# Optimization experiments

Measured on AMD Instinct MI355X. Metric: run time of the kernel, lower is better.

Reference implementation:

```python
import jax, jax.numpy as jnp
import numpy as np

DIMS = (8, 8, 16, 16)   # 4D lattice, X = prod(DIMS) = 16384
KS = 2                  # kernel_size
DIL = 0                 # dilation
NC = 3                  # SU(3)
N_IN = 4
N_OUT = 8
T_W_SIZE = N_IN * (2 * (KS - 1) * len(DIMS) + 1) + 1  # 37 (includes unit element)
BATCH = 4
X = int(np.prod(DIMS))


def complex_einsum(pattern, a, b, conj_a=1, conj_b=1):
    # last axis of a, b is (real, imag)
    aR, aI = a[..., 0], conj_a * a[..., 1]
    bR, bI = b[..., 0], conj_b * b[..., 1]
    cR = jnp.einsum(pattern, aR, bR) - jnp.einsum(pattern, aI, bI)
    cI = jnp.einsum(pattern, aR, bI) + jnp.einsum(pattern, aI, bR)
    return jnp.stack((cR, cI), axis=-1)


def shift(a, axis, orientation):
    # roll the flattened lattice dim X along lattice axis `axis`
    s = a.shape
    a_l = a.reshape((s[0],) + DIMS + s[2:])
    return jnp.roll(a_l, orientation, axis=axis + 1).reshape(s)


def transport(u, w, axis, orientation):
    ws = shift(w, axis, -orientation)
    ua = u[:, :, axis]  # (b, X, nc, nc, 2)
    if orientation > 0:
        wt = complex_einsum('bxij,bxwjk->bxwik', ua, ws)
        wt = complex_einsum('bxwij,bxkj->bxwik', wt, ua, conj_b=-1)
    else:
        ua = shift(ua, axis, +1)
        wt = complex_einsum('bxji,bxwjk->bxwik', ua, ws, conj_a=-1)
        wt = complex_einsum('bxwij,bxjk->bxwik', wt, ua)
    return wt


def setup_inputs() -> dict:
    key = jax.random.key(0)
    k1, k2, k3 = jax.random.split(key, 3)
    u = jax.random.normal(k1, (BATCH, X, len(DIMS), NC, NC, 2), dtype=jnp.float32)
    w = jax.random.normal(k2, (BATCH, X, N_IN, NC, NC, 2), dtype=jnp.float32)
    std = 1.0 * float(np.sqrt(1.0 / T_W_SIZE))
    weight = std * jax.random.normal(k3, (N_OUT, T_W_SIZE), dtype=jnp.float32)
    return {"u": u, "w": w, "weight": weight}


def reference(u, w, weight):
    terms = [w]
    for orientation in (+1, -1):
        for axis in range(len(DIMS)):
            wt = w
            for d in range(1, KS):
                for step in range(DIL + 1):
                    wt = transport(u, wt, axis=axis, orientation=orientation)
                terms.append(wt)
    t_w = jnp.concatenate(terms, axis=2)  # (b, X, n_in*(2*(ks-1)*ndim+1), nc, nc, 2)
    # append unit (identity) element channel
    unit = jnp.stack((jnp.eye(NC, dtype=t_w.dtype), jnp.zeros((NC, NC), dtype=t_w.dtype)), axis=-1)
    unit_t = jnp.broadcast_to(unit, (t_w.shape[0], t_w.shape[1], 1, NC, NC, 2))
    t_w = jnp.concatenate((t_w, unit_t), axis=2)  # (b, X, T_W_SIZE, nc, nc, 2)
    w_out = jnp.einsum('uv,bxvijc->bxuijc', weight, t_w)
    return (u, w_out)
```

## Files before the change

kernel.cpp:

```cpp
#include <hip/hip_runtime.h>

namespace {

constexpr int NCOL  = 3;
constexpr int N_IN  = 4;
constexpr int N_OUT = 8;
constexpr int T_W   = 37;
constexpr int NB    = 4;
constexpr int NX    = 16384;
constexpr int MAT   = 18;
constexpr int NSJ   = NB * NX * 3;
constexpr int NTHREADS = NSJ * 2;
constexpr int OUT_U = NB * NX * 4 * MAT;

__device__ constexpr int SH[4] = {11, 8, 4, 0};
__device__ constexpr int DD[4] = {8, 8, 16, 16};
__device__ constexpr int SS[4] = {2048, 256, 16, 1};

template<int PAR>
__device__ __forceinline__ void load_mat18(const float* __restrict__ p, float* M) {
    if constexpr (PAR == 0) {
        float4 q0 = *(const float4*)(p + 0);
        float4 q1 = *(const float4*)(p + 4);
        float4 q2 = *(const float4*)(p + 8);
        float4 q3 = *(const float4*)(p + 12);
        float2 q4 = *(const float2*)(p + 16);
        M[0]=q0.x;  M[1]=q0.y;  M[2]=q0.z;  M[3]=q0.w;
        M[4]=q1.x;  M[5]=q1.y;  M[6]=q1.z;  M[7]=q1.w;
        M[8]=q2.x;  M[9]=q2.y;  M[10]=q2.z; M[11]=q2.w;
        M[12]=q3.x; M[13]=q3.y; M[14]=q3.z; M[15]=q3.w;
        M[16]=q4.x; M[17]=q4.y;
    } else {
        float2 q4 = *(const float2*)(p + 0);
        float4 q0 = *(const float4*)(p + 2);
        float4 q1 = *(const float4*)(p + 6);
        float4 q2 = *(const float4*)(p + 10);
        float4 q3 = *(const float4*)(p + 14);
        M[0]=q4.x;  M[1]=q4.y;
        M[2]=q0.x;  M[3]=q0.y;  M[4]=q0.z;  M[5]=q0.w;
        M[6]=q1.x;  M[7]=q1.y;  M[8]=q1.z;  M[9]=q1.w;
        M[10]=q2.x; M[11]=q2.y; M[12]=q2.z; M[13]=q2.w;
        M[14]=q3.x; M[15]=q3.y; M[16]=q3.z; M[17]=q3.w;
    }
}

template<int O>
__device__ __forceinline__ void transport_col(
    const float U[18], const float vr[3], const float vi[3],
    const float W[18], float cr[3], float ci[3])
{
    float yr[3], yi[3];
#pragma unroll
    for (int i = 0; i < 3; ++i) {
        float sr = 0.f, si = 0.f;
#pragma unroll
        for (int k = 0; k < 3; ++k) {
            float wr = W[(i*3+k)*2], wi = W[(i*3+k)*2+1];
            sr = fmaf(wr, vr[k], sr); sr = fmaf(-wi, vi[k], sr);
            si = fmaf(wr, vi[k], si); si = fmaf(wi, vr[k], si);
        }
        yr[i] = sr; yi[i] = si;
    }
#pragma unroll
    for (int i = 0; i < 3; ++i) {
        float sr = 0.f, si = 0.f;
#pragma unroll
        for (int k = 0; k < 3; ++k) {
            if constexpr (O == 0) {
                float ur = U[(i*3+k)*2], ui = U[(i*3+k)*2+1];
                sr = fmaf(ur, yr[k], sr); sr = fmaf(-ui, yi[k], sr);
                si = fmaf(ur, yi[k], si); si = fmaf(ui, yr[k], si);
            } else {
                float ur = U[(k*3+i)*2], ui = U[(k*3+i)*2+1];
                sr = fmaf(ur, yr[k], sr); sr = fmaf(ui, yi[k], sr);
                si = fmaf(ur, yi[k], si); si = fmaf(-ui, yr[k], si);
            }
        }
        cr[i] = sr; ci[i] = si;
    }
}

__device__ __forceinline__ void mix(const float (*wT)[N_OUT], int ch,
    const float cr[3], const float ci[3], float acc[N_OUT][NCOL][2])
{
    float4 lo = *(const float4*)&wT[ch][0];
    float4 hi = *(const float4*)&wT[ch][4];
    const float cw[8] = {lo.x, lo.y, lo.z, lo.w, hi.x, hi.y, hi.z, hi.w};
#pragma unroll
    for (int uo = 0; uo < 8; ++uo)
#pragma unroll
        for (int i = 0; i < 3; ++i) {
            acc[uo][i][0] = fmaf(cw[uo], cr[i], acc[uo][i][0]);
            acc[uo][i][1] = fmaf(cw[uo], ci[i], acc[uo][i][1]);
        }
}

template<int O>
__device__ __forceinline__ void do_orientation(
    int x, int bs, int j,
    const float* __restrict__ u, const float* __restrict__ w,
    const float (*wT)[N_OUT], float acc[N_OUT][NCOL][2])
{
#pragma unroll
    for (int a = 0; a < 4; ++a) {
        const int ca = (x >> SH[a]) & (DD[a] - 1);
        int xn;
        if constexpr (O == 0) xn = (ca == DD[a]-1) ? x - (DD[a]-1)*SS[a] : x + SS[a];
        else                  xn = (ca == 0)       ? x + (DD[a]-1)*SS[a] : x - SS[a];
        const int bsn = bs - x + xn;
        const int us  = (O == 0) ? bs : bsn;

        const float* __restrict__ Up = u + (size_t)us * (4 * MAT) + a * MAT;
        float U[18];
        if ((a & 1) == 0) load_mat18<0>(Up, U);
        else              load_mat18<1>(Up, U);

        float vr[3], vi[3];
#pragma unroll
        for (int k = 0; k < 3; ++k) {
            const int eidx = (O == 0) ? (j*3 + k) : (k*3 + j);
            float2 e = *(const float2*)(Up + eidx * 2);
            vr[k] = e.x;
            vi[k] = (O == 0) ? -e.y : e.y;
        }

        const float* __restrict__ wn = w + (size_t)bsn * (N_IN * MAT);
        const int chbase = ((O == 0) ? (1 + a) : (5 + a)) * 4;

        float WA[18], WB[18], cr[3], ci[3];
        load_mat18<0>(wn + 0 * MAT, WA);
        load_mat18<1>(wn + 1 * MAT, WB);

        transport_col<O>(U, vr, vi, WA, cr, ci);
        mix(wT, chbase + 0, cr, ci, acc);
        load_mat18<0>(wn + 2 * MAT, WA);

        transport_col<O>(U, vr, vi, WB, cr, ci);
        mix(wT, chbase + 1, cr, ci, acc);
        load_mat18<1>(wn + 3 * MAT, WB);

        transport_col<O>(U, vr, vi, WA, cr, ci);
        mix(wT, chbase + 2, cr, ci, acc);

        transport_col<O>(U, vr, vi, WB, cr, ci);
        mix(wT, chbase + 3, cr, ci, acc);
    }
}

__global__ __launch_bounds__(256) void lconv_kernel(
    const float* __restrict__ u,
    const float* __restrict__ w,
    const float* __restrict__ wgt,
    float* __restrict__ out)
{
    __shared__ float  wT[T_W][N_OUT];
    __shared__ float2 red[256][13];

    const int tid = threadIdx.x;
    for (int idx = tid; idx < T_W * N_OUT; idx += 256) {
        int uo = idx & 7;
        int v  = idx >> 3;
        wT[v][uo] = wgt[uo * T_W + v];
    }
    __syncthreads();

    const int gid = blockIdx.x * 256 + tid;

    {
        const float4* __restrict__ u4 = (const float4*)u;
        float4* __restrict__ o4 = (float4*)out;
#pragma unroll
        for (int k = 0; k < 3; ++k) {
            int idx = gid + k * NTHREADS;
            o4[idx] = u4[idx];
        }
    }

    const int o  = tid >> 7;
    const int sj = blockIdx.x * 128 + (tid & 127);
    const int j  = sj % 3;
    const int bs = sj / 3;
    const int x  = bs & (NX - 1);

    const float* __restrict__ wbase = w + (size_t)bs * (N_IN * MAT);

    float acc[N_OUT][NCOL][2];
#pragma unroll
    for (int uo = 0; uo < N_OUT; ++uo)
#pragma unroll
        for (int i = 0; i < NCOL; ++i) { acc[uo][i][0] = 0.f; acc[uo][i][1] = 0.f; }

#pragma unroll
    for (int t = 0; t < 2; ++t) {
        const int v = 2 * o + t;
        float4 lo = *(const float4*)&wT[v][0];
        float4 hi = *(const float4*)&wT[v][4];
        const float cw[8] = {lo.x, lo.y, lo.z, lo.w, hi.x, hi.y, hi.z, hi.w};
#pragma unroll
        for (int i = 0; i < NCOL; ++i) {
            float2 e = *(const float2*)(wbase + v * MAT + (i * NCOL + j) * 2);
#pragma unroll
            for (int uo = 0; uo < N_OUT; ++uo) {
                acc[uo][i][0] = fmaf(cw[uo], e.x, acc[uo][i][0]);
                acc[uo][i][1] = fmaf(cw[uo], e.y, acc[uo][i][1]);
            }
        }
    }

    if (o == 0) do_orientation<0>(x, bs, j, u, w, wT, acc);
    else        do_orientation<1>(x, bs, j, u, w, wT, acc);

    if (o == 0) {
#pragma unroll
        for (int t = 0; t < 4; ++t)
#pragma unroll
            for (int i = 0; i < 3; ++i)
                red[tid][t * 3 + i] = make_float2(acc[4 + t][i][0], acc[4 + t][i][1]);
    } else {
#pragma unroll
        for (int t = 0; t < 4; ++t)
#pragma unroll
            for (int i = 0; i < 3; ++i)
                red[tid][t * 3 + i] = make_float2(acc[t][i][0], acc[t][i][1]);
    }
    __syncthreads();

    const int partner = tid ^ 128;
    float* __restrict__ obase = out + (size_t)OUT_U + (size_t)bs * (N_OUT * MAT);
    float4 idq = *(const float4*)&wT[36][4 * o];
    const float cid[4] = {idq.x, idq.y, idq.z, idq.w};

    if (o == 0) {
#pragma unroll
        for (int t = 0; t < 4; ++t)
#pragma unroll
            for (int i = 0; i < 3; ++i) {
                float2 r = red[partner][t * 3 + i];
                float2 e;
                e.x = acc[t][i][0] + r.x + ((i == j) ? cid[t] : 0.f);
                e.y = acc[t][i][1] + r.y;
                *(float2*)(obase + t * MAT + (i * NCOL + j) * 2) = e;
            }
    } else {
#pragma unroll
        for (int t = 0; t < 4; ++t)
#pragma unroll
            for (int i = 0; i < 3; ++i) {
                float2 r = red[partner][t * 3 + i];
                float2 e;
                e.x = acc[4 + t][i][0] + r.x + ((i == j) ? cid[t] : 0.f);
                e.y = acc[4 + t][i][1] + r.y;
                *(float2*)(obase + (4 + t) * MAT + (i * NCOL + j) * 2) = e;
            }
    }
}

}

extern "C" void kernel_launch(void* const* d_in, const int* in_sizes, int n_in,
                              void* d_out, int out_size, void* d_ws, size_t ws_size,
                              hipStream_t stream)
{
    const float* u   = (const float*)d_in[0];
    const float* w   = (const float*)d_in[1];
    const float* wgt = (const float*)d_in[2];
    float* out = (float*)d_out;

    dim3 block(256);
    dim3 grid(NTHREADS / 256);
    lconv_kernel<<<grid, block, 0, stream>>>(u, w, wgt, out);
}
```

Baseline: 57.23 us.

## Remap threads so each wavefront handles one column across 64 sites

Blocks grow to 384 threads covering 64 sites. Each wavefront now owns one (orientation, column) pair, so the column index and orientation are uniform within a wavefront and the branching on j no longer diverges. The column vector for the link matrix is now taken from the matrix already held in registers instead of being reloaded from memory. The cross-orientation reduction uses a smaller shared buffer and is done in two phases with extra barriers, which adds synchronisation. Per-lane loads of neighbouring sites become more contiguous.

```diff
diff --git a/kernel.cpp b/kernel.cpp
--- a/kernel.cpp
+++ b/kernel.cpp
@@ -9,9 +9,11 @@
 constexpr int NB    = 4;
 constexpr int NX    = 16384;
 constexpr int MAT   = 18;
-constexpr int NSJ   = NB * NX * 3;
-constexpr int NTHREADS = NSJ * 2;
-constexpr int OUT_U = NB * NX * 4 * MAT;
+constexpr int SITES = NB * NX;
+constexpr int BLK   = 384;
+constexpr int NBLK  = SITES / 64;
+constexpr int NTHREADS = NBLK * BLK;
+constexpr int OUT_U = SITES * 4 * MAT;
 
 __device__ constexpr int SH[4] = {11, 8, 4, 0};
 __device__ constexpr int DD[4] = {8, 8, 16, 16};
@@ -44,6 +46,15 @@
     }
 }
 
+template<int O, int J>
+__device__ __forceinline__ void extract_d(const float U[18], float vr[3], float vi[3]) {
+#pragma unroll
+    for (int k = 0; k < 3; ++k) {
+        if constexpr (O == 0) { vr[k] = U[(J*3+k)*2]; vi[k] = -U[(J*3+k)*2+1]; }
+        else                  { vr[k] = U[(k*3+J)*2]; vi[k] =  U[(k*3+J)*2+1]; }
+    }
+}
+
 template<int O>
 __device__ __forceinline__ void transport_col(
     const float U[18], const float vr[3], const float vi[3],
@@ -116,13 +127,9 @@
         else              load_mat18<1>(Up, U);
 
         float vr[3], vi[3];
-#pragma unroll
-        for (int k = 0; k < 3; ++k) {
-            const int eidx = (O == 0) ? (j*3 + k) : (k*3 + j);
-            float2 e = *(const float2*)(Up + eidx * 2);
-            vr[k] = e.x;
-            vi[k] = (O == 0) ? -e.y : e.y;
-        }
+        if      (j == 0) extract_d<O, 0>(U, vr, vi);
+        else if (j == 1) extract_d<O, 1>(U, vr, vi);
+        else             extract_d<O, 2>(U, vr, vi);
 
         const float* __restrict__ wn = w + (size_t)bsn * (N_IN * MAT);
         const int chbase = ((O == 0) ? (1 + a) : (5 + a)) * 4;
@@ -147,24 +154,22 @@
     }
 }
 
-__global__ __launch_bounds__(256) void lconv_kernel(
+__global__ __launch_bounds__(BLK) void lconv_kernel(
     const float* __restrict__ u,
     const float* __restrict__ w,
     const float* __restrict__ wgt,
     float* __restrict__ out)
 {
     __shared__ float  wT[T_W][N_OUT];
-    __shared__ float2 red[256][13];
+    __shared__ float2 red[192][13];
 
     const int tid = threadIdx.x;
-    for (int idx = tid; idx < T_W * N_OUT; idx += 256) {
-        int uo = idx & 7;
-        int v  = idx >> 3;
-        wT[v][uo] = wgt[uo * T_W + v];
-    }
-    __syncthreads();
-
-    const int gid = blockIdx.x * 256 + tid;
+    for (int idx = tid; idx < T_W * N_OUT; idx += BLK) {
+        wT[idx >> 3][idx & 7] = wgt[(idx & 7) * T_W + (idx >> 3)];
+    }
+    __syncthreads();
+
+    const int gid = blockIdx.x * BLK + tid;
 
     {
         const float4* __restrict__ u4 = (const float4*)u;
@@ -176,11 +181,12 @@
         }
     }
 
-    const int o  = tid >> 7;
-    const int sj = blockIdx.x * 128 + (tid & 127);
-    const int j  = sj % 3;
-    const int bs = sj / 3;
-    const int x  = bs & (NX - 1);
+    const int wv   = tid >> 6;
+    const int lane = tid & 63;
+    const int o    = (wv >= 3) ? 1 : 0;
+    const int j    = wv - 3 * o;
+    const int bs   = blockIdx.x * 64 + lane;
+    const int x    = bs & (NX - 1);
 
     const float* __restrict__ wbase = w + (size_t)bs * (N_IN * MAT);
 
@@ -210,43 +216,47 @@
     if (o == 0) do_orientation<0>(x, bs, j, u, w, wT, acc);
     else        do_orientation<1>(x, bs, j, u, w, wT, acc);
 
-    if (o == 0) {
-#pragma unroll
-        for (int t = 0; t < 4; ++t)
-#pragma unroll
-            for (int i = 0; i < 3; ++i)
-                red[tid][t * 3 + i] = make_float2(acc[4 + t][i][0], acc[4 + t][i][1]);
-    } else {
-#pragma unroll
-        for (int t = 0; t < 4; ++t)
-#pragma unroll
-            for (int i = 0; i < 3; ++i)
-                red[tid][t * 3 + i] = make_float2(acc[t][i][0], acc[t][i][1]);
-    }
-    __syncthreads();
-
-    const int partner = tid ^ 128;
+    const int p = tid - 192 * o;
     float* __restrict__ obase = out + (size_t)OUT_U + (size_t)bs * (N_OUT * MAT);
     float4 idq = *(const float4*)&wT[36][4 * o];
     const float cid[4] = {idq.x, idq.y, idq.z, idq.w};
 
+    if (o == 1) {
+#pragma unroll
+        for (int t = 0; t < 4; ++t)
+#pragma unroll
+            for (int i = 0; i < 3; ++i)
+                red[p][t * 3 + i] = make_float2(acc[t][i][0], acc[t][i][1]);
+    }
+    __syncthreads();
     if (o == 0) {
 #pragma unroll
         for (int t = 0; t < 4; ++t)
 #pragma unroll
             for (int i = 0; i < 3; ++i) {
-                float2 r = red[partner][t * 3 + i];
+                float2 r = red[p][t * 3 + i];
                 float2 e;
                 e.x = acc[t][i][0] + r.x + ((i == j) ? cid[t] : 0.f);
                 e.y = acc[t][i][1] + r.y;
                 *(float2*)(obase + t * MAT + (i * NCOL + j) * 2) = e;
             }
-    } else {
+    }
+    __syncthreads();
+
+    if (o == 0) {
+#pragma unroll
+        for (int t = 0; t < 4; ++t)
+#pragma unroll
+            for (int i = 0; i < 3; ++i)
+                red[p][t * 3 + i] = make_float2(acc[4 + t][i][0], acc[4 + t][i][1]);
+    }
+    __syncthreads();
+    if (o == 1) {
 #pragma unroll
         for (int t = 0; t < 4; ++t)
 #pragma unroll
             for (int i = 0; i < 3; ++i) {
-                float2 r = red[partner][t * 3 + i];
+                float2 r = red[p][t * 3 + i];
                 float2 e;
                 e.x = acc[4 + t][i][0] + r.x + ((i == j) ? cid[t] : 0.f);
                 e.y = acc[4 + t][i][1] + r.y;
@@ -266,7 +276,7 @@
     const float* wgt = (const float*)d_in[2];
     float* out = (float*)d_out;
 
-    dim3 block(256);
-    dim3 grid(NTHREADS / 256);
+    dim3 block(BLK);
+    dim3 grid(NBLK);
     lconv_kernel<<<grid, block, 0, stream>>>(u, w, wgt, out);
 }
```

After: 184.0 us. 3.22x slower.
